# Performance work log

Measured on AMD Instinct MI355X. Metric: run time of the kernel, lower is better.

## Reference

```python
import jax, jax.numpy as jnp
import numpy as np

N = 40000        # num nodes
E = 640000       # num edges
F_IN = 512
F_OUT = 32
HEADS = 8
NEG_SLOPE = 0.2
EPS = 1e-16


def setup_inputs() -> dict:
    key = jax.random.key(0)
    k1, k2, k3, k4, k5 = jax.random.split(key, 5)
    x = jax.random.normal(k1, (N, F_IN), dtype=jnp.float32)
    edge_index = jax.random.randint(k2, (2, E), 0, N, dtype=jnp.int32)
    # xavier-uniform-like init scales
    lim_W = float(np.sqrt(6.0 / (F_IN + F_OUT)))
    lim_a = float(np.sqrt(6.0 / (HEADS + F_OUT)))
    W = jax.random.uniform(k3, (HEADS, F_IN, F_OUT), dtype=jnp.float32, minval=-lim_W, maxval=lim_W)
    a_src = jax.random.uniform(k4, (HEADS, F_OUT), dtype=jnp.float32, minval=-lim_a, maxval=lim_a)
    a_dst = jax.random.uniform(k5, (HEADS, F_OUT), dtype=jnp.float32, minval=-lim_a, maxval=lim_a)
    bias = jnp.zeros((HEADS * F_OUT,), dtype=jnp.float32)
    return {"x": x, "edge_index": edge_index, "W": W, "a_src": a_src, "a_dst": a_dst, "bias": bias}


def reference(x, edge_index, W, a_src, a_dst, bias):
    src, dst = edge_index[0], edge_index[1]
    # per-head projection: [N, H, F_out]
    h = jnp.einsum('nd,hdf->nhf', x, W)
    # attention logit pieces computed per-node then gathered per-edge
    # (same math as gathering h then dotting with a)
    s_src = jnp.einsum('nhf,hf->nh', h, a_src)   # [N, H]
    s_dst = jnp.einsum('nhf,hf->nh', h, a_dst)   # [N, H]
    e = s_src[src] + s_dst[dst]                  # [E, H]
    e = jnp.where(e >= 0, e, NEG_SLOPE * e)      # LeakyReLU(0.2)
    # edge softmax over incoming edges of each dst node (global max shift, as in source)
    e = e - jnp.max(e)
    exp_e = jnp.exp(e)
    denom = jax.ops.segment_sum(exp_e, dst, num_segments=N)   # [N, H]
    alpha = exp_e / (denom[dst] + EPS)                        # [E, H]
    # weighted message aggregation (dropout is identity in eval / p=0)
    msg = alpha[..., None] * h[src]                           # [E, H, F_out]
    out = jax.ops.segment_sum(msg, dst, num_segments=N)       # [N, H, F_out]
    out = out.reshape(N, HEADS * F_OUT) + bias                # concat=True
    return out
```

## Files before the change

### kernel.cpp

```cpp
#include <hip/hip_runtime.h>
#include <hip/hip_bf16.h>
#include <math.h>
#include <stdint.h>

#define N_NODES 40000
#define N_EDGES 640000
#define F_IN    512
#define F_OUT   32
#define HEADS   8
#define C_OUT   (HEADS * F_OUT)
#define NEG_SLOPE 0.2f
#define EPS_F   1e-16f

typedef __attribute__((ext_vector_type(8)))  short  short8;
typedef __attribute__((ext_vector_type(4)))  short  short4v;
typedef __attribute__((ext_vector_type(16))) float  float16v;

__device__ __forceinline__ void splitT(float f, unsigned short& hi, unsigned short& lo) {
    unsigned u = __float_as_uint(f);
    hi = (unsigned short)(u >> 16);
    float r = f - __uint_as_float(u & 0xFFFF0000u);
    lo = (unsigned short)(__float_as_uint(r) >> 16);
}

__device__ __forceinline__ unsigned short f2bf(float f) {
    unsigned u = __float_as_uint(f);
    return (unsigned short)((u + 0x7FFF + ((u >> 16) & 1)) >> 16);
}

__global__ __launch_bounds__(256) void pack_and_count(const float* __restrict__ W,
                                                      unsigned short* __restrict__ Bp,
                                                      const int* __restrict__ dst,
                                                      int* __restrict__ count) {
    if (blockIdx.x < 512) {
        int tid = blockIdx.x * 256 + threadIdx.x;
        int j    = tid & 7;
        int L    = (tid >> 3) & 63;
        int ni   = (tid >> 9) & 1;
        int ktg  = (tid >> 10) & 31;
        int wc   = tid >> 15;
        int k    = ktg * 16 + (L >> 5) * 8 + j;
        int col  = wc * 64 + ni * 32 + (L & 31);
        int hh = col >> 5, f = col & 31;
        Bp[tid] = f2bf(W[hh * (F_IN * F_OUT) + k * F_OUT + f]);
    } else {
        int e = (blockIdx.x - 512) * 256 + threadIdx.x;
        atomicAdd(&count[dst[e]], 1);
    }
}

#define AS 66

__global__ __launch_bounds__(512, 4) void gemm_mfma(const float* __restrict__ x,
                                                    const unsigned short* __restrict__ Bp,
                                                    const float* __restrict__ a_src,
                                                    const float* __restrict__ a_dst,
                                                    unsigned short* __restrict__ h16,
                                                    float* __restrict__ s_src,
                                                    float* __restrict__ s_dst) {
    __shared__ unsigned short As_hi[64 * AS];
    __shared__ unsigned short As_lo[64 * AS];

    const int t = threadIdx.x;
    const int wave = t >> 6, L = t & 63;
    const int wr = wave & 1, wc = wave >> 1;
    const int r31 = L & 31, half = L >> 5;
    const int n0 = blockIdx.x * 64;

    float16v acc[2];
#pragma unroll
    for (int ni = 0; ni < 2; ++ni)
#pragma unroll
        for (int r = 0; r < 16; ++r) acc[ni][r] = 0.f;

    const int kcol = (t & 15) * 4;
    const int rbase = t >> 4;

    float4 stg[2][2];
#pragma unroll
    for (int it = 0; it < 2; ++it)
        stg[0][it] = *(const float4*)&x[(size_t)(n0 + rbase + it * 32) * F_IN + kcol];

#pragma unroll
    for (int st = 0; st < 8; ++st) {
        const int cur = st & 1, nxt = cur ^ 1;
        __syncthreads();

        if (st < 7) {
            const int kb2 = (st + 1) * 64;
#pragma unroll
            for (int it = 0; it < 2; ++it)
                stg[nxt][it] = *(const float4*)&x[(size_t)(n0 + rbase + it * 32) * F_IN + kb2 + kcol];
        }

#pragma unroll
        for (int it = 0; it < 2; ++it) {
            float4 v = stg[cur][it];
            unsigned short h0, h1, h2, h3, l0, l1, l2, l3;
            splitT(v.x, h0, l0); splitT(v.y, h1, l1);
            splitT(v.z, h2, l2); splitT(v.w, h3, l3);
            int off = (rbase + it * 32) * AS + kcol;
            *(short4v*)&As_hi[off] = (short4v){(short)h0, (short)h1, (short)h2, (short)h3};
            *(short4v*)&As_lo[off] = (short4v){(short)l0, (short)l1, (short)l2, (short)l3};
        }
        __syncthreads();

        short8 breg[4][2];
#pragma unroll
        for (int kt = 0; kt < 4; ++kt)
#pragma unroll
            for (int ni = 0; ni < 2; ++ni) {
                size_t idx = ((((size_t)wc * 32 + (st * 4 + kt)) * 2 + ni) * 64 + L) * 8;
                breg[kt][ni] = *(const short8*)&Bp[idx];
            }

#pragma unroll
        for (int kt = 0; kt < 4; ++kt) {
            int off = (wr * 32 + r31) * AS + kt * 16 + half * 8;
            short8 ah = *(const short8*)&As_hi[off];
            short8 al = *(const short8*)&As_lo[off];
#pragma unroll
            for (int ni = 0; ni < 2; ++ni) {
                acc[ni] = __builtin_amdgcn_mfma_f32_32x32x16_bf16(ah, breg[kt][ni], acc[ni], 0, 0, 0);
                acc[ni] = __builtin_amdgcn_mfma_f32_32x32x16_bf16(al, breg[kt][ni], acc[ni], 0, 0, 0);
            }
        }
    }

#pragma unroll
    for (int ni = 0; ni < 2; ++ni) {
        int colb = wc * 64 + ni * 32 + r31;
#pragma unroll
        for (int r = 0; r < 16; ++r) {
            int row = n0 + wr * 32 + (r & 3) + 8 * (r >> 2) + 4 * half;
            h16[(size_t)row * C_OUT + colb] = f2bf(acc[ni][r]);
        }
    }

#pragma unroll
    for (int ni = 0; ni < 2; ++ni) {
        int hh = wc * 2 + ni;
        float af = a_src[hh * 32 + r31];
        float df = a_dst[hh * 32 + r31];
#pragma unroll
        for (int r = 0; r < 16; ++r) {
            float v = acc[ni][r];
            float vs = v * af;
            float vd = v * df;
#pragma unroll
            for (int m = 1; m < 32; m <<= 1) {
                vs += __shfl_xor(vs, m, 64);
                vd += __shfl_xor(vd, m, 64);
            }
            if (r31 == 0) {
                int row = n0 + wr * 32 + (r & 3) + 8 * (r >> 2) + 4 * half;
                s_src[row * 8 + hh] = vs;
                s_dst[row * 8 + hh] = vd;
            }
        }
    }
}

__global__ __launch_bounds__(1024) void scan_local(const int* __restrict__ count,
                                                   int* __restrict__ row_excl,
                                                   int* __restrict__ cursor,
                                                   int* __restrict__ btot) {
    __shared__ int woff[16];
    __shared__ int tot_s;
    const int b = blockIdx.x, t = threadIdx.x;
    const int lane = t & 63, wid = t >> 6;
    const int i = b * 1000 + t;
    int v = (t < 1000) ? count[i] : 0;
    int inc = v;
#pragma unroll
    for (int d = 1; d < 64; d <<= 1) {
        int u = __shfl_up(inc, d, 64);
        if (lane >= d) inc += u;
    }
    if (lane == 63) woff[wid] = inc;
    __syncthreads();
    if (t < 16) {
        int s = woff[t];
        int sc = s;
#pragma unroll
        for (int d = 1; d < 16; d <<= 1) {
            int u = __shfl_up(sc, d, 64);
            if (t >= d) sc += u;
        }
        woff[t] = sc - s;
        if (t == 15) tot_s = sc;
    }
    __syncthreads();
    int excl = woff[wid] + inc - v;
    if (t < 1000) { row_excl[i] = excl; cursor[i] = excl; }
    if (t == 0) btot[b] = tot_s;
}

__global__ __launch_bounds__(64) void scan_tots(const int* __restrict__ btot,
                                                int* __restrict__ boff) {
    const int t = threadIdx.x;
    int v = (t < 40) ? btot[t] : 0;
    int inc = v;
#pragma unroll
    for (int d = 1; d < 64; d <<= 1) {
        int u = __shfl_up(inc, d, 64);
        if (t >= d) inc += u;
    }
    if (t < 40) boff[t] = inc - v;
}

__global__ __launch_bounds__(256) void scatter_edges(const int* __restrict__ src,
                                                     const int* __restrict__ dst,
                                                     int* __restrict__ cursor,
                                                     const int* __restrict__ boff,
                                                     int* __restrict__ src_sorted) {
    int e = blockIdx.x * 256 + threadIdx.x;
    int s = src[e], d = dst[e];
    int pos = atomicAdd(&cursor[d], 1) + boff[d / 1000];
    src_sorted[pos] = s;
}

__global__ __launch_bounds__(256) void aggregate(const int* __restrict__ src_sorted,
                                                 const unsigned short* __restrict__ h16,
                                                 const float* __restrict__ s_src,
                                                 const float* __restrict__ s_dst,
                                                 const int* __restrict__ row_excl,
                                                 const int* __restrict__ boff,
                                                 const int* __restrict__ count,
                                                 const float* __restrict__ bias,
                                                 float* __restrict__ out) {
    const int t = threadIdx.x;
    const int wave = t >> 6, lane = t & 63;
    const int wgid = blockIdx.x * 4 + wave;
    const int ch0 = lane * 4;
    const int hh = lane >> 3;

    auto bf2f = [](short v) { return __uint_as_float(((unsigned)(unsigned short)v) << 16); };
    const float4 b4 = *(const float4*)&bias[ch0];

    for (int n = wgid; n < N_NODES; n += 8192) {
        const int start = row_excl[n] + boff[n / 1000];
        const int cnt = count[n];
        const float sd = s_dst[n * 8 + hh];

        float a0 = 0.f, a1 = 0.f, a2 = 0.f, a3 = 0.f, den = 0.f;

        int base = 0;
        for (; base + 8 <= cnt; base += 8) {
            int idx = start + base;
            int s[8];
#pragma unroll
            for (int u = 0; u < 8; ++u)
                s[u] = src_sorted[idx + u];

            short4v v[8];
#pragma unroll
            for (int u = 0; u < 8; ++u)
                v[u] = *(const short4v*)&h16[(size_t)s[u] * C_OUT + ch0];

            float w[8];
#pragma unroll
            for (int u = 0; u < 8; ++u) {
                float e = s_src[s[u] * 8 + hh] + sd;
                e = e >= 0.f ? e : NEG_SLOPE * e;
                w[u] = __expf(e);
            }

#pragma unroll
            for (int u = 0; u < 8; ++u) {
                a0 += w[u] * bf2f(v[u][0]);
                a1 += w[u] * bf2f(v[u][1]);
                a2 += w[u] * bf2f(v[u][2]);
                a3 += w[u] * bf2f(v[u][3]);
                den += w[u];
            }
        }

        int rem = cnt - base;
        if (rem > 0) {
            int idx = start + base;
            int s[8];
#pragma unroll
            for (int u = 0; u < 8; ++u)
                s[u] = (u < rem) ? src_sorted[idx + u] : 0;

            short4v v[8];
#pragma unroll
            for (int u = 0; u < 8; ++u)
                v[u] = *(const short4v*)&h16[(size_t)s[u] * C_OUT + ch0];

            float w[8];
#pragma unroll
            for (int u = 0; u < 8; ++u) {
                float e = s_src[s[u] * 8 + hh] + sd;
                e = e >= 0.f ? e : NEG_SLOPE * e;
                w[u] = (u < rem) ? __expf(e) : 0.f;
            }

#pragma unroll
            for (int u = 0; u < 8; ++u) {
                a0 += w[u] * bf2f(v[u][0]);
                a1 += w[u] * bf2f(v[u][1]);
                a2 += w[u] * bf2f(v[u][2]);
                a3 += w[u] * bf2f(v[u][3]);
                den += w[u];
            }
        }

        float inv = 1.0f / (den + EPS_F);
        float4 o;
        o.x = a0 * inv + b4.x;
        o.y = a1 * inv + b4.y;
        o.z = a2 * inv + b4.z;
        o.w = a3 * inv + b4.w;
        *(float4*)&out[(size_t)n * C_OUT + ch0] = o;
    }
}

extern "C" void kernel_launch(void* const* d_in, const int* in_sizes, int n_in,
                              void* d_out, int out_size, void* d_ws, size_t ws_size,
                              hipStream_t stream) {
    const float* x     = (const float*)d_in[0];
    const int*   eidx  = (const int*)d_in[1];
    const float* W     = (const float*)d_in[2];
    const float* a_src = (const float*)d_in[3];
    const float* a_dst = (const float*)d_in[4];
    const float* bias  = (const float*)d_in[5];
    float* out = (float*)d_out;

    const int* src = eidx;
    const int* dst = eidx + N_EDGES;

    char* p = (char*)d_ws;
    auto carve = [&](size_t bytes) {
        char* r = p;
        p += (bytes + 255) & ~(size_t)255;
        return r;
    };
    unsigned short* h16 = (unsigned short*)carve((size_t)N_NODES * C_OUT * 2);
    float* s_src      = (float*)carve((size_t)N_NODES * HEADS * 4);
    float* s_dst      = (float*)carve((size_t)N_NODES * HEADS * 4);
    int*   src_sorted = (int*)carve((size_t)N_EDGES * 4);
    int*   count      = (int*)carve((size_t)N_NODES * 4);
    int*   row_excl   = (int*)carve((size_t)N_NODES * 4);
    int*   cursor     = (int*)carve((size_t)N_NODES * 4);
    int*   btot       = (int*)carve(64 * 4);
    int*   boff       = (int*)carve(64 * 4);
    unsigned short* Bp = (unsigned short*)carve((size_t)131072 * 2);

    hipMemsetAsync(count, 0, (size_t)N_NODES * 4, stream);

    pack_and_count<<<512 + N_EDGES / 256, 256, 0, stream>>>(W, Bp, dst, count);
    gemm_mfma<<<625, 512, 0, stream>>>(x, Bp, a_src, a_dst, h16, s_src, s_dst);
    scan_local<<<40, 1024, 0, stream>>>(count, row_excl, cursor, btot);
    scan_tots<<<1, 64, 0, stream>>>(btot, boff);
    scatter_edges<<<N_EDGES / 256, 256, 0, stream>>>(src, dst, cursor, boff, src_sorted);
    aggregate<<<2048, 256, 0, stream>>>(src_sorted, h16, s_src, s_dst,
                                        row_excl, boff, count, bias, out);
}
```

Before: 300.3 us.

## Shrink GEMM tile to 32 rows and double-buffer LDS with one barrier per stage

The GEMM block is halved to 32 rows and 256 threads, so each wave computes 32 rows by 64 columns and the grid doubles to 1250 blocks. The LDS A tile is now double-buffered. Global loads run two stages ahead and the hi/lo split conversion for the next stage happens after the MFMAs, which removes the second __syncthreads per iteration. The aim is more blocks for load balancing and better overlap of x loads and conversion with MFMA work, at the cost of each B fragment being reused across fewer rows, so B is read from global memory twice as often.

```diff
diff --git a/kernel.cpp b/kernel.cpp
--- a/kernel.cpp
+++ b/kernel.cpp
@@ -51,21 +51,20 @@
 
 #define AS 66
 
-__global__ __launch_bounds__(512, 4) void gemm_mfma(const float* __restrict__ x,
+__global__ __launch_bounds__(256, 4) void gemm_mfma(const float* __restrict__ x,
                                                     const unsigned short* __restrict__ Bp,
                                                     const float* __restrict__ a_src,
                                                     const float* __restrict__ a_dst,
                                                     unsigned short* __restrict__ h16,
                                                     float* __restrict__ s_src,
                                                     float* __restrict__ s_dst) {
-    __shared__ unsigned short As_hi[64 * AS];
-    __shared__ unsigned short As_lo[64 * AS];
+    __shared__ unsigned short As_hi[2][32 * AS];
+    __shared__ unsigned short As_lo[2][32 * AS];
 
     const int t = threadIdx.x;
-    const int wave = t >> 6, L = t & 63;
-    const int wr = wave & 1, wc = wave >> 1;
+    const int wc = t >> 6, L = t & 63;
     const int r31 = L & 31, half = L >> 5;
-    const int n0 = blockIdx.x * 64;
+    const int n0 = blockIdx.x * 32;
 
     float16v acc[2];
 #pragma unroll
@@ -75,36 +74,37 @@
 
     const int kcol = (t & 15) * 4;
     const int rbase = t >> 4;
+    const float* xr0 = &x[(size_t)(n0 + rbase) * F_IN + kcol];
+    const float* xr1 = &x[(size_t)(n0 + rbase + 16) * F_IN + kcol];
+
+#define CONVW(b, s0, s1) do {                                                  \
+        unsigned short h0,h1,h2,h3,l0,l1,l2,l3;                                \
+        splitT((s0).x,h0,l0); splitT((s0).y,h1,l1);                            \
+        splitT((s0).z,h2,l2); splitT((s0).w,h3,l3);                            \
+        *(short4v*)&As_hi[b][rbase*AS + kcol] =                                \
+            (short4v){(short)h0,(short)h1,(short)h2,(short)h3};                \
+        *(short4v*)&As_lo[b][rbase*AS + kcol] =                                \
+            (short4v){(short)l0,(short)l1,(short)l2,(short)l3};                \
+        splitT((s1).x,h0,l0); splitT((s1).y,h1,l1);                            \
+        splitT((s1).z,h2,l2); splitT((s1).w,h3,l3);                            \
+        *(short4v*)&As_hi[b][(rbase+16)*AS + kcol] =                           \
+            (short4v){(short)h0,(short)h1,(short)h2,(short)h3};                \
+        *(short4v*)&As_lo[b][(rbase+16)*AS + kcol] =                           \
+            (short4v){(short)l0,(short)l1,(short)l2,(short)l3};                \
+    } while (0)
 
     float4 stg[2][2];
-#pragma unroll
-    for (int it = 0; it < 2; ++it)
-        stg[0][it] = *(const float4*)&x[(size_t)(n0 + rbase + it * 32) * F_IN + kcol];
+    stg[0][0] = *(const float4*)(xr0);
+    stg[0][1] = *(const float4*)(xr1);
+    CONVW(0, stg[0][0], stg[0][1]);
+    stg[1][0] = *(const float4*)(xr0 + 64);
+    stg[1][1] = *(const float4*)(xr1 + 64);
 
 #pragma unroll
     for (int st = 0; st < 8; ++st) {
         const int cur = st & 1, nxt = cur ^ 1;
         __syncthreads();
 
-        if (st < 7) {
-            const int kb2 = (st + 1) * 64;
-#pragma unroll
-            for (int it = 0; it < 2; ++it)
-                stg[nxt][it] = *(const float4*)&x[(size_t)(n0 + rbase + it * 32) * F_IN + kb2 + kcol];
-        }
-
-#pragma unroll
-        for (int it = 0; it < 2; ++it) {
-            float4 v = stg[cur][it];
-            unsigned short h0, h1, h2, h3, l0, l1, l2, l3;
-            splitT(v.x, h0, l0); splitT(v.y, h1, l1);
-            splitT(v.z, h2, l2); splitT(v.w, h3, l3);
-            int off = (rbase + it * 32) * AS + kcol;
-            *(short4v*)&As_hi[off] = (short4v){(short)h0, (short)h1, (short)h2, (short)h3};
-            *(short4v*)&As_lo[off] = (short4v){(short)l0, (short)l1, (short)l2, (short)l3};
-        }
-        __syncthreads();
-
         short8 breg[4][2];
 #pragma unroll
         for (int kt = 0; kt < 4; ++kt)
@@ -114,25 +114,33 @@
                 breg[kt][ni] = *(const short8*)&Bp[idx];
             }
 
+        if (st < 6) {
+            stg[cur][0] = *(const float4*)(xr0 + (st + 2) * 64);
+            stg[cur][1] = *(const float4*)(xr1 + (st + 2) * 64);
+        }
+
 #pragma unroll
         for (int kt = 0; kt < 4; ++kt) {
-            int off = (wr * 32 + r31) * AS + kt * 16 + half * 8;
-            short8 ah = *(const short8*)&As_hi[off];
-            short8 al = *(const short8*)&As_lo[off];
+            int off = r31 * AS + kt * 16 + half * 8;
+            short8 ah = *(const short8*)&As_hi[cur][off];
+            short8 al = *(const short8*)&As_lo[cur][off];
 #pragma unroll
             for (int ni = 0; ni < 2; ++ni) {
                 acc[ni] = __builtin_amdgcn_mfma_f32_32x32x16_bf16(ah, breg[kt][ni], acc[ni], 0, 0, 0);
                 acc[ni] = __builtin_amdgcn_mfma_f32_32x32x16_bf16(al, breg[kt][ni], acc[ni], 0, 0, 0);
             }
         }
-    }
+
+        if (st < 7) CONVW(nxt, stg[nxt][0], stg[nxt][1]);
+    }
+#undef CONVW
 
 #pragma unroll
     for (int ni = 0; ni < 2; ++ni) {
         int colb = wc * 64 + ni * 32 + r31;
 #pragma unroll
         for (int r = 0; r < 16; ++r) {
-            int row = n0 + wr * 32 + (r & 3) + 8 * (r >> 2) + 4 * half;
+            int row = n0 + (r & 3) + 8 * (r >> 2) + 4 * half;
             h16[(size_t)row * C_OUT + colb] = f2bf(acc[ni][r]);
         }
     }
@@ -153,7 +161,7 @@
                 vd += __shfl_xor(vd, m, 64);
             }
             if (r31 == 0) {
-                int row = n0 + wr * 32 + (r & 3) + 8 * (r >> 2) + 4 * half;
+                int row = n0 + (r & 3) + 8 * (r >> 2) + 4 * half;
                 s_src[row * 8 + hh] = vs;
                 s_dst[row * 8 + hh] = vd;
             }
@@ -351,7 +359,7 @@
     hipMemsetAsync(count, 0, (size_t)N_NODES * 4, stream);
 
     pack_and_count<<<512 + N_EDGES / 256, 256, 0, stream>>>(W, Bp, dst, count);
-    gemm_mfma<<<625, 512, 0, stream>>>(x, Bp, a_src, a_dst, h16, s_src, s_dst);
+    gemm_mfma<<<1250, 256, 0, stream>>>(x, Bp, a_src, a_dst, h16, s_src, s_dst);
     scan_local<<<40, 1024, 0, stream>>>(count, row_excl, cursor, btot);
     scan_tots<<<1, 64, 0, stream>>>(btot, boff);
     scatter_edges<<<N_EDGES / 256, 256, 0, stream>>>(src, dst, cursor, boff, src_sorted);
```

Result: no change. 298.0 us (-0.8%).
